# Kernel optimization log

Measured on AMD Instinct MI355X. Metric: run time of the kernel, lower is better.

## Reference

```python
import jax, jax.numpy as jnp
import numpy as np

N = 100000   # nodes
E = 1600000  # edges
D_IN = 64    # latent_dim
D_H = 64     # hidden_channels
D_OUT = 3    # coord_dim
EPS = 1e-5


def layer_norm(x, g, b):
    mu = jnp.mean(x, axis=-1, keepdims=True)
    var = jnp.mean(jnp.square(x - mu), axis=-1, keepdims=True)
    return (x - mu) * jax.lax.rsqrt(var + EPS) * g + b


def gcn_conv(x, W, b, src, dst, n):
    # PyG GCNConv: h = x W; symmetric norm deg^-1/2 (self-loops already in src/dst)
    h = x @ W  # [N, F]
    ones = jnp.ones(src.shape[0], dtype=h.dtype)
    deg = jax.ops.segment_sum(ones, dst, num_segments=n)
    dinv = jnp.where(deg > 0, jax.lax.rsqrt(deg), 0.0)
    coef = (dinv[src] * dinv[dst])[:, None]  # [E, 1]
    out = jax.ops.segment_sum(h[src] * coef, dst, num_segments=n)  # scatter-add
    return out + b


def setup_inputs() -> dict:
    key = jax.random.key(0)
    ks = jax.random.split(key, 10)
    z = jax.random.normal(ks[0], (N, D_IN), dtype=jnp.float32)
    edge_index = jax.random.randint(ks[1], (2, E), 0, N, dtype=jnp.int64)
    s = 1.0 / np.sqrt(D_H)
    return {
        "z": z,
        "edge_index": edge_index,
        "W1": jax.random.normal(ks[2], (D_IN, D_H), jnp.float32) * s,
        "b1": jnp.zeros((D_H,), jnp.float32),
        "g1": jnp.ones((D_H,), jnp.float32),
        "beta1": jnp.zeros((D_H,), jnp.float32),
        "W2": jax.random.normal(ks[3], (D_H, D_H), jnp.float32) * s,
        "b2": jnp.zeros((D_H,), jnp.float32),
        "g2": jnp.ones((D_H,), jnp.float32),
        "beta2": jnp.zeros((D_H,), jnp.float32),
        "Wm1": jax.random.normal(ks[4], (D_H, D_H), jnp.float32) * s,
        "bm1": jnp.zeros((D_H,), jnp.float32),
        "Wm2": jax.random.normal(ks[5], (D_H, D_OUT), jnp.float32) * s,
        "bm2": jnp.zeros((D_OUT,), jnp.float32),
    }


def reference(z, edge_index, W1, b1, g1, beta1, W2, b2, g2, beta2, Wm1, bm1, Wm2, bm2):
    n = z.shape[0]
    loops = jnp.arange(n, dtype=edge_index.dtype)
    src = jnp.concatenate([edge_index[0], loops])
    dst = jnp.concatenate([edge_index[1], loops])
    h = layer_norm(jax.nn.relu(gcn_conv(z, W1, b1, src, dst, n)), g1, beta1)
    h = layer_norm(jax.nn.relu(gcn_conv(h, W2, b2, src, dst, n)), g2, beta2)
    h = jax.nn.relu(h @ Wm1 + bm1)
    return h @ Wm2 + bm2
```

## Files before the change

### kernel.cpp

```cpp
#include <hip/hip_runtime.h>
#include <hip/hip_bf16.h>

#define LN_EPS 1e-5f
#define EPB 4096
typedef unsigned short u16;
typedef unsigned short us8 __attribute__((ext_vector_type(8)));
typedef short s8v __attribute__((ext_vector_type(8)));
typedef float f32x4 __attribute__((ext_vector_type(4)));

static __device__ __forceinline__ float bf2f(u16 x) {
    return __uint_as_float(((unsigned int)x) << 16);
}
static __device__ __forceinline__ u16 f2bf(float f) {
    unsigned int u = __float_as_uint(f);
    return (u16)((u + 0x7fff + ((u >> 16) & 1)) >> 16);
}

__global__ __launch_bounds__(256) void k_p1_hist(const int* __restrict__ dst,
                                                 int* __restrict__ blockhist,
                                                 int E, int NB) {
    extern __shared__ int h[];
    int b = blockIdx.x, t = threadIdx.x;
    for (int j = t; j < NB; j += 256) h[j] = 0;
    __syncthreads();
    int e0 = b * EPB, e1 = min(E, e0 + EPB);
    for (int e = e0 + t; e < e1; e += 256)
        atomicAdd(&h[dst[e] >> 8], 1);
    __syncthreads();
    for (int j = t; j < NB; j += 256)
        blockhist[(size_t)b * NB + j] = h[j];
}

__global__ __launch_bounds__(512) void k_p2a(int* __restrict__ blockhist,
                                             int* __restrict__ btot, int NB, int NB1) {
    __shared__ int sd[512];
    int k = blockIdx.x, t = threadIdx.x;
    int v = (t < NB1) ? blockhist[(size_t)t * NB + k] : 0;
    sd[t] = v;
    __syncthreads();
    for (int off = 1; off < 512; off <<= 1) {
        int x = (t >= off) ? sd[t - off] : 0;
        __syncthreads();
        sd[t] += x;
        __syncthreads();
    }
    if (t < NB1) blockhist[(size_t)t * NB + k] = sd[t] - v;
    if (t == 511) btot[k] = sd[511];
}

__global__ __launch_bounds__(512) void k_p2b(const int* __restrict__ btot,
                                             int* __restrict__ bbase,
                                             int* __restrict__ row_ptr,
                                             int NB, int N, int E) {
    __shared__ int sd[512];
    int t = threadIdx.x;
    int v = (t < NB) ? btot[t] : 0;
    sd[t] = v;
    __syncthreads();
    for (int off = 1; off < 512; off <<= 1) {
        int x = (t >= off) ? sd[t - off] : 0;
        __syncthreads();
        sd[t] += x;
        __syncthreads();
    }
    if (t < NB) bbase[t] = sd[t] - v;
    if (t == 0) { bbase[NB] = E; row_ptr[N] = E; }
}

__global__ __launch_bounds__(256) void k_p3_scatter(const int* __restrict__ src,
                                                    const int* __restrict__ dst,
                                                    const int* __restrict__ blockhist,
                                                    const int* __restrict__ bbase,
                                                    int* __restrict__ entries,
                                                    int E, int NB) {
    extern __shared__ int cur[];
    int b = blockIdx.x, t = threadIdx.x;
    for (int j = t; j < NB; j += 256)
        cur[j] = bbase[j] + blockhist[(size_t)b * NB + j];
    __syncthreads();
    int e0 = b * EPB, e1 = min(E, e0 + EPB);
    for (int e = e0 + t; e < e1; e += 256) {
        int d = dst[e];
        int p = atomicAdd(&cur[d >> 8], 1);
        entries[p] = (src[e] << 8) | (d & 255);
    }
}

__global__ __launch_bounds__(256) void k_p4_csr(const int* __restrict__ entries,
                                                const int* __restrict__ bbase,
                                                int* __restrict__ row_ptr,
                                                float* __restrict__ dinv,
                                                int* __restrict__ csr_src, int N) {
    __shared__ int hist[256];
    __shared__ int sd[256];
    __shared__ int cur[256];
    int k = blockIdx.x, t = threadIdx.x;
    int b0 = bbase[k], b1 = bbase[k + 1];
    hist[t] = 0;
    __syncthreads();
    for (int e = b0 + t; e < b1; e += 256)
        atomicAdd(&hist[entries[e] & 255], 1);
    __syncthreads();
    int v = hist[t];
    sd[t] = v;
    __syncthreads();
    for (int off = 1; off < 256; off <<= 1) {
        int x = (t >= off) ? sd[t - off] : 0;
        __syncthreads();
        sd[t] += x;
        __syncthreads();
    }
    int excl = sd[t] - v;
    int node = (k << 8) + t;
    if (node < N) {
        row_ptr[node] = b0 + excl;
        dinv[node] = rsqrtf(1.0f + (float)v);
    }
    cur[t] = b0 + excl;
    __syncthreads();
    for (int e = b0 + t; e < b1; e += 256) {
        int en = entries[e];
        int p = atomicAdd(&cur[en & 255], 1);
        csr_src[p] = en >> 8;
    }
}

__global__ __launch_bounds__(256) void k_prep_w(const float* __restrict__ W1,
                                                const float* __restrict__ W2,
                                                const float* __restrict__ Wm1,
                                                u16* __restrict__ Wtb) {
    int idx = blockIdx.x * 256 + threadIdx.x;
    if (idx >= 3 * 4096) return;
    int m = idx >> 12;
    int kc = idx & 4095;
    int col = kc >> 6, k = kc & 63;
    const float* W = (m == 0) ? W1 : (m == 1) ? W2 : Wm1;
    Wtb[idx] = f2bf(W[k * 64 + col]);
}

template <bool A_FP32>
__global__ __launch_bounds__(256) void k_mfma_gemm(const void* __restrict__ A_,
                                                   const u16* __restrict__ Wtb,
                                                   const float* __restrict__ dinv,
                                                   u16* __restrict__ C, int N) {
    int tid = threadIdx.x;
    int wid = tid >> 6, l = tid & 63;
    int li = l & 15, hi = l >> 4;
    int n0 = blockIdx.x * 64 + wid * 16;
    if (n0 >= N) return;
    int k0 = hi * 8;

    s8v a[2];
    int nr = min(n0 + li, N - 1);
    if (A_FP32) {
        const float* A = (const float*)A_;
        #pragma unroll
        for (int kk = 0; kk < 2; ++kk) {
            const float* p = A + (size_t)nr * 64 + kk * 32 + k0;
            float4 f0 = *reinterpret_cast<const float4*>(p);
            float4 f1 = *reinterpret_cast<const float4*>(p + 4);
            a[kk][0] = (short)f2bf(f0.x); a[kk][1] = (short)f2bf(f0.y);
            a[kk][2] = (short)f2bf(f0.z); a[kk][3] = (short)f2bf(f0.w);
            a[kk][4] = (short)f2bf(f1.x); a[kk][5] = (short)f2bf(f1.y);
            a[kk][6] = (short)f2bf(f1.z); a[kk][7] = (short)f2bf(f1.w);
        }
    } else {
        const u16* A = (const u16*)A_;
        #pragma unroll
        for (int kk = 0; kk < 2; ++kk)
            a[kk] = *reinterpret_cast<const s8v*>(A + (size_t)nr * 64 + kk * 32 + k0);
    }

    s8v b[4][2];
    #pragma unroll
    for (int ct = 0; ct < 4; ++ct)
        #pragma unroll
        for (int kk = 0; kk < 2; ++kk)
            b[ct][kk] = *reinterpret_cast<const s8v*>(Wtb + (ct * 16 + li) * 64 + kk * 32 + k0);

    f32x4 acc[4] = {{0.f, 0.f, 0.f, 0.f}, {0.f, 0.f, 0.f, 0.f},
                    {0.f, 0.f, 0.f, 0.f}, {0.f, 0.f, 0.f, 0.f}};
    #pragma unroll
    for (int kk = 0; kk < 2; ++kk)
        #pragma unroll
        for (int ct = 0; ct < 4; ++ct)
            acc[ct] = __builtin_amdgcn_mfma_f32_16x16x32_bf16(a[kk], b[ct][kk], acc[ct], 0, 0, 0);

    float dv[4];
    #pragma unroll
    for (int r = 0; r < 4; ++r) {
        int node = n0 + hi * 4 + r;
        dv[r] = (node < N) ? dinv[node] : 0.f;
    }
    #pragma unroll
    for (int ct = 0; ct < 4; ++ct)
        #pragma unroll
        for (int r = 0; r < 4; ++r) {
            int node = n0 + hi * 4 + r;
            if (node < N)
                C[(size_t)node * 64 + ct * 16 + li] = f2bf(acc[ct][r] * dv[r]);
        }
}

__global__ __launch_bounds__(256) void k_mfma_mlp(const u16* __restrict__ A,
                                                  const u16* __restrict__ Wtb,
                                                  const float* __restrict__ bm1,
                                                  const float* __restrict__ Wm2,
                                                  const float* __restrict__ bm2,
                                                  float* __restrict__ out, int N) {
    int tid = threadIdx.x;
    int wid = tid >> 6, l = tid & 63;
    int li = l & 15, hi = l >> 4;
    int n0 = blockIdx.x * 64 + wid * 16;
    if (n0 >= N) return;
    int k0 = hi * 8;

    s8v a[2];
    int nr = min(n0 + li, N - 1);
    #pragma unroll
    for (int kk = 0; kk < 2; ++kk)
        a[kk] = *reinterpret_cast<const s8v*>(A + (size_t)nr * 64 + kk * 32 + k0);

    s8v b[4][2];
    #pragma unroll
    for (int ct = 0; ct < 4; ++ct)
        #pragma unroll
        for (int kk = 0; kk < 2; ++kk)
            b[ct][kk] = *reinterpret_cast<const s8v*>(Wtb + (ct * 16 + li) * 64 + kk * 32 + k0);

    f32x4 acc[4] = {{0.f, 0.f, 0.f, 0.f}, {0.f, 0.f, 0.f, 0.f},
                    {0.f, 0.f, 0.f, 0.f}, {0.f, 0.f, 0.f, 0.f}};
    #pragma unroll
    for (int kk = 0; kk < 2; ++kk)
        #pragma unroll
        for (int ct = 0; ct < 4; ++ct)
            acc[ct] = __builtin_amdgcn_mfma_f32_16x16x32_bf16(a[kk], b[ct][kk], acc[ct], 0, 0, 0);

    float p[4][3];
    #pragma unroll
    for (int r = 0; r < 4; ++r)
        #pragma unroll
        for (int c = 0; c < 3; ++c) p[r][c] = 0.f;

    #pragma unroll
    for (int ct = 0; ct < 4; ++ct) {
        int col = ct * 16 + li;
        float bb = bm1[col];
        float w0 = Wm2[col * 3 + 0], w1 = Wm2[col * 3 + 1], w2 = Wm2[col * 3 + 2];
        #pragma unroll
        for (int r = 0; r < 4; ++r) {
            float v = fmaxf(acc[ct][r] + bb, 0.f);
            p[r][0] += v * w0;
            p[r][1] += v * w1;
            p[r][2] += v * w2;
        }
    }
    #pragma unroll
    for (int off = 1; off < 16; off <<= 1)
        #pragma unroll
        for (int r = 0; r < 4; ++r)
            #pragma unroll
            for (int c = 0; c < 3; ++c)
                p[r][c] += __shfl_xor(p[r][c], off);

    if (li == 0) {
        float o0 = bm2[0], o1 = bm2[1], o2 = bm2[2];
        #pragma unroll
        for (int r = 0; r < 4; ++r) {
            int node = n0 + hi * 4 + r;
            if (node < N) {
                out[(size_t)node * 3 + 0] = p[r][0] + o0;
                out[(size_t)node * 3 + 1] = p[r][1] + o1;
                out[(size_t)node * 3 + 2] = p[r][2] + o2;
            }
        }
    }
}

__global__ __launch_bounds__(256) void k_gather_ln(const u16* __restrict__ Hb,
                                                   const int* __restrict__ row_ptr,
                                                   const int* __restrict__ csr_src,
                                                   const float* __restrict__ dinv,
                                                   const float* __restrict__ b,
                                                   const float* __restrict__ g,
                                                   const float* __restrict__ beta,
                                                   u16* __restrict__ outb, int N) {
    int tid = blockIdx.x * blockDim.x + threadIdx.x;
    int node = tid >> 3;
    if (node >= N) return;
    int fl = threadIdx.x & 7;
    const us8* H8 = reinterpret_cast<const us8*>(Hb);

    float a[8];
    #pragma unroll
    for (int k = 0; k < 8; ++k) a[k] = 0.f;

    int beg = row_ptr[node], end = row_ptr[node + 1];
    int j = beg;
    for (; j + 2 <= end; j += 2) {
        int s0 = csr_src[j];
        int s1 = csr_src[j + 1];
        us8 h0 = H8[(size_t)s0 * 8 + fl];
        us8 h1 = H8[(size_t)s1 * 8 + fl];
        #pragma unroll
        for (int k = 0; k < 8; ++k)
            a[k] += bf2f(h0[k]) + bf2f(h1[k]);
    }
    if (j < end) {
        int s0 = csr_src[j];
        us8 h0 = H8[(size_t)s0 * 8 + fl];
        #pragma unroll
        for (int k = 0; k < 8; ++k)
            a[k] += bf2f(h0[k]);
    }
    float dd = dinv[node];
    {
        us8 hs = H8[(size_t)node * 8 + fl];
        #pragma unroll
        for (int k = 0; k < 8; ++k)
            a[k] += bf2f(hs[k]);
    }
    #pragma unroll
    for (int k = 0; k < 8; ++k) a[k] *= dd;

    float4 b0 = *reinterpret_cast<const float4*>(b + fl * 8);
    float4 b1v = *reinterpret_cast<const float4*>(b + fl * 8 + 4);
    a[0] = fmaxf(a[0] + b0.x, 0.f); a[1] = fmaxf(a[1] + b0.y, 0.f);
    a[2] = fmaxf(a[2] + b0.z, 0.f); a[3] = fmaxf(a[3] + b0.w, 0.f);
    a[4] = fmaxf(a[4] + b1v.x, 0.f); a[5] = fmaxf(a[5] + b1v.y, 0.f);
    a[6] = fmaxf(a[6] + b1v.z, 0.f); a[7] = fmaxf(a[7] + b1v.w, 0.f);

    float s = 0.f;
    #pragma unroll
    for (int k = 0; k < 8; ++k) s += a[k];
    s += __shfl_xor(s, 1); s += __shfl_xor(s, 2); s += __shfl_xor(s, 4);
    float mu = s * (1.0f / 64.0f);
    float vs = 0.f;
    #pragma unroll
    for (int k = 0; k < 8; ++k) {
        float d = a[k] - mu;
        vs += d * d;
    }
    vs += __shfl_xor(vs, 1); vs += __shfl_xor(vs, 2); vs += __shfl_xor(vs, 4);
    float r = rsqrtf(vs * (1.0f / 64.0f) + LN_EPS);

    float4 g0 = *reinterpret_cast<const float4*>(g + fl * 8);
    float4 g1 = *reinterpret_cast<const float4*>(g + fl * 8 + 4);
    float4 e0 = *reinterpret_cast<const float4*>(beta + fl * 8);
    float4 e1 = *reinterpret_cast<const float4*>(beta + fl * 8 + 4);
    us8 o;
    o[0] = f2bf((a[0] - mu) * r * g0.x + e0.x);
    o[1] = f2bf((a[1] - mu) * r * g0.y + e0.y);
    o[2] = f2bf((a[2] - mu) * r * g0.z + e0.z);
    o[3] = f2bf((a[3] - mu) * r * g0.w + e0.w);
    o[4] = f2bf((a[4] - mu) * r * g1.x + e1.x);
    o[5] = f2bf((a[5] - mu) * r * g1.y + e1.y);
    o[6] = f2bf((a[6] - mu) * r * g1.z + e1.z);
    o[7] = f2bf((a[7] - mu) * r * g1.w + e1.w);
    *reinterpret_cast<us8*>(outb + (size_t)node * 64 + fl * 8) = o;
}

extern "C" void kernel_launch(void* const* d_in, const int* in_sizes, int n_in,
                              void* d_out, int out_size, void* d_ws, size_t ws_size,
                              hipStream_t stream) {
    const float* z     = (const float*)d_in[0];
    const int*   ei    = (const int*)d_in[1];
    const float* W1    = (const float*)d_in[2];
    const float* b1    = (const float*)d_in[3];
    const float* g1    = (const float*)d_in[4];
    const float* beta1 = (const float*)d_in[5];
    const float* W2    = (const float*)d_in[6];
    const float* b2    = (const float*)d_in[7];
    const float* g2    = (const float*)d_in[8];
    const float* beta2 = (const float*)d_in[9];
    const float* Wm1   = (const float*)d_in[10];
    const float* bm1   = (const float*)d_in[11];
    const float* Wm2   = (const float*)d_in[12];
    const float* bm2   = (const float*)d_in[13];

    int N = in_sizes[0] / 64;
    int E = in_sizes[1] / 2;
    const int* src = ei;
    const int* dst = ei + E;
    float* out = (float*)d_out;

    int NB  = (N + 255) >> 8;
    int NB1 = (E + EPB - 1) / EPB;

    size_t N64 = (size_t)N * 64;
    auto rnd = [](size_t x) { return (x + 1023) & ~(size_t)1023; };
    int*   bbase     = (int*)d_ws;
    int*   btot      = bbase + rnd(NB + 1);
    int*   blockhist = btot + rnd(NB);
    int*   entries   = blockhist + rnd((size_t)NB1 * NB);
    int*   row_ptr   = entries + rnd(E);
    float* dinv      = (float*)(row_ptr + rnd(N + 1));
    int*   csr_src   = (int*)(dinv + rnd(N));
    u16*   Hb        = (u16*)(csr_src + rnd(E));
    u16*   Hb2       = Hb + rnd(N64);
    u16*   Wtb       = Hb2 + rnd(N64);

    int nb_g = (N + 63) / 64;
    int nb_gw = (N * 8 + 255) / 256;
    size_t lds_nb = (size_t)NB * sizeof(int);

    k_prep_w<<<48, 256, 0, stream>>>(W1, W2, Wm1, Wtb);
    k_p1_hist<<<NB1, 256, lds_nb, stream>>>(dst, blockhist, E, NB);
    k_p2a<<<NB, 512, 0, stream>>>(blockhist, btot, NB, NB1);
    k_p2b<<<1, 512, 0, stream>>>(btot, bbase, row_ptr, NB, N, E);
    k_p3_scatter<<<NB1, 256, lds_nb, stream>>>(src, dst, blockhist, bbase, entries, E, NB);
    k_p4_csr<<<NB, 256, 0, stream>>>(entries, bbase, row_ptr, dinv, csr_src, N);

    k_mfma_gemm<true><<<nb_g, 256, 0, stream>>>(z, Wtb, dinv, Hb, N);
    k_gather_ln<<<nb_gw, 256, 0, stream>>>(Hb, row_ptr, csr_src, dinv, b1, g1, beta1, Hb2, N);
    k_mfma_gemm<false><<<nb_g, 256, 0, stream>>>(Hb2, Wtb + 4096, dinv, Hb, N);
    k_gather_ln<<<nb_gw, 256, 0, stream>>>(Hb, row_ptr, csr_src, dinv, b2, g2, beta2, Hb2, N);
    k_mfma_mlp<<<nb_g, 256, 0, stream>>>(Hb2, Wtb + 8192, bm1, Wm2, bm2, out, N);
}
```

Before: 168.1 us.

## Split features into quarter-planes for gather and fuse layernorm into following GEMM

Stores the post-GEMM features as four planes of 16 features each ([4][N][16] bf16), and runs the gather once per plane, so each plane's 3.2MB working set fits better in cache. The gather now only sums raw neighbour features. The dinv scale, bias, ReLU and layernorm move into the A-fragment loading of the next GEMM or MLP kernel. The weight-prep kernel is folded into the p2b scan launch to remove one launch. The cost is four times as many CSR index reads in the gather and a cross-lane LN reduction inside the GEMM kernels.

After: 227.0 us. 1.35x slower.

```diff
diff --git a/kernel.cpp b/kernel.cpp
--- a/kernel.cpp
+++ b/kernel.cpp
@@ -4,6 +4,7 @@
 #define LN_EPS 1e-5f
 #define EPB 4096
 typedef unsigned short u16;
+typedef unsigned short us4 __attribute__((ext_vector_type(4)));
 typedef unsigned short us8 __attribute__((ext_vector_type(8)));
 typedef short s8v __attribute__((ext_vector_type(8)));
 typedef float f32x4 __attribute__((ext_vector_type(4)));
@@ -48,23 +49,38 @@
     if (t == 511) btot[k] = sd[511];
 }
 
-__global__ __launch_bounds__(512) void k_p2b(const int* __restrict__ btot,
-                                             int* __restrict__ bbase,
-                                             int* __restrict__ row_ptr,
-                                             int NB, int N, int E) {
-    __shared__ int sd[512];
-    int t = threadIdx.x;
-    int v = (t < NB) ? btot[t] : 0;
-    sd[t] = v;
-    __syncthreads();
-    for (int off = 1; off < 512; off <<= 1) {
-        int x = (t >= off) ? sd[t - off] : 0;
+__global__ __launch_bounds__(512) void k_p2b_prep(const int* __restrict__ btot,
+                                                  int* __restrict__ bbase,
+                                                  int* __restrict__ row_ptr,
+                                                  int NB, int N, int E,
+                                                  const float* __restrict__ W1,
+                                                  const float* __restrict__ W2,
+                                                  const float* __restrict__ Wm1,
+                                                  u16* __restrict__ Wtb) {
+    if (blockIdx.x == 0) {
+        __shared__ int sd[512];
+        int t = threadIdx.x;
+        int v = (t < NB) ? btot[t] : 0;
+        sd[t] = v;
         __syncthreads();
-        sd[t] += x;
-        __syncthreads();
-    }
-    if (t < NB) bbase[t] = sd[t] - v;
-    if (t == 0) { bbase[NB] = E; row_ptr[N] = E; }
+        for (int off = 1; off < 512; off <<= 1) {
+            int x = (t >= off) ? sd[t - off] : 0;
+            __syncthreads();
+            sd[t] += x;
+            __syncthreads();
+        }
+        if (t < NB) bbase[t] = sd[t] - v;
+        if (t == 0) { bbase[NB] = E; row_ptr[N] = E; }
+    } else {
+        int idx = (blockIdx.x - 1) * 512 + threadIdx.x;
+        if (idx < 3 * 4096) {
+            int m = idx >> 12;
+            int kc = idx & 4095;
+            int col = kc >> 6, k = kc & 63;
+            const float* W = (m == 0) ? W1 : (m == 1) ? W2 : Wm1;
+            Wtb[idx] = f2bf(W[k * 64 + col]);
+        }
+    }
 }
 
 __global__ __launch_bounds__(256) void k_p3_scatter(const int* __restrict__ src,
@@ -125,24 +141,53 @@
     }
 }
 
-__global__ __launch_bounds__(256) void k_prep_w(const float* __restrict__ W1,
-                                                const float* __restrict__ W2,
-                                                const float* __restrict__ Wm1,
-                                                u16* __restrict__ Wtb) {
-    int idx = blockIdx.x * 256 + threadIdx.x;
-    if (idx >= 3 * 4096) return;
-    int m = idx >> 12;
-    int kc = idx & 4095;
-    int col = kc >> 6, k = kc & 63;
-    const float* W = (m == 0) ? W1 : (m == 1) ? W2 : Wm1;
-    Wtb[idx] = f2bf(W[k * 64 + col]);
-}
-
-template <bool A_FP32>
-__global__ __launch_bounds__(256) void k_mfma_gemm(const void* __restrict__ A_,
-                                                   const u16* __restrict__ Wtb,
-                                                   const float* __restrict__ dinv,
-                                                   u16* __restrict__ C, int N) {
+static __device__ __forceinline__ void ln_frags(const u16* __restrict__ AGQ, size_t N,
+                                                int nr, int hi,
+                                                const float* __restrict__ dinv,
+                                                const float* __restrict__ bias,
+                                                const float* __restrict__ g,
+                                                const float* __restrict__ beta,
+                                                s8v a[2]) {
+    float dd = dinv[nr];
+    int qlo = hi >> 1, off = (hi & 1) * 8;
+    us8 lo = *reinterpret_cast<const us8*>(AGQ + ((size_t)qlo * N + nr) * 16 + off);
+    us8 hv = *reinterpret_cast<const us8*>(AGQ + ((size_t)(2 + qlo) * N + nr) * 16 + off);
+    float v[16];
+    #pragma unroll
+    for (int j = 0; j < 8; ++j) {
+        v[j] = bf2f(lo[j]) * dd;
+        v[8 + j] = bf2f(hv[j]) * dd;
+    }
+    int f0 = hi * 8;
+    #pragma unroll
+    for (int j = 0; j < 8; ++j) {
+        v[j] = fmaxf(v[j] + bias[f0 + j], 0.f);
+        v[8 + j] = fmaxf(v[8 + j] + bias[32 + f0 + j], 0.f);
+    }
+    float s = 0.f;
+    #pragma unroll
+    for (int j = 0; j < 16; ++j) s += v[j];
+    s += __shfl_xor(s, 16); s += __shfl_xor(s, 32);
+    float mu = s * (1.0f / 64.0f);
+    float vs = 0.f;
+    #pragma unroll
+    for (int j = 0; j < 16; ++j) {
+        float d = v[j] - mu;
+        vs += d * d;
+    }
+    vs += __shfl_xor(vs, 16); vs += __shfl_xor(vs, 32);
+    float r = rsqrtf(vs * (1.0f / 64.0f) + LN_EPS);
+    #pragma unroll
+    for (int j = 0; j < 8; ++j) {
+        a[0][j] = (short)f2bf((v[j] - mu) * r * g[f0 + j] + beta[f0 + j]);
+        a[1][j] = (short)f2bf((v[8 + j] - mu) * r * g[32 + f0 + j] + beta[32 + f0 + j]);
+    }
+}
+
+__global__ __launch_bounds__(256) void k_gemm1(const float* __restrict__ A,
+                                               const u16* __restrict__ Wtb,
+                                               const float* __restrict__ dinv,
+                                               u16* __restrict__ C, int N) {
     int tid = threadIdx.x;
     int wid = tid >> 6, l = tid & 63;
     int li = l & 15, hi = l >> 4;
@@ -152,23 +197,15 @@
 
     s8v a[2];
     int nr = min(n0 + li, N - 1);
-    if (A_FP32) {
-        const float* A = (const float*)A_;
-        #pragma unroll
-        for (int kk = 0; kk < 2; ++kk) {
-            const float* p = A + (size_t)nr * 64 + kk * 32 + k0;
-            float4 f0 = *reinterpret_cast<const float4*>(p);
-            float4 f1 = *reinterpret_cast<const float4*>(p + 4);
-            a[kk][0] = (short)f2bf(f0.x); a[kk][1] = (short)f2bf(f0.y);
-            a[kk][2] = (short)f2bf(f0.z); a[kk][3] = (short)f2bf(f0.w);
-            a[kk][4] = (short)f2bf(f1.x); a[kk][5] = (short)f2bf(f1.y);
-            a[kk][6] = (short)f2bf(f1.z); a[kk][7] = (short)f2bf(f1.w);
-        }
-    } else {
-        const u16* A = (const u16*)A_;
-        #pragma unroll
-        for (int kk = 0; kk < 2; ++kk)
-            a[kk] = *reinterpret_cast<const s8v*>(A + (size_t)nr * 64 + kk * 32 + k0);
+    #pragma unroll
+    for (int kk = 0; kk < 2; ++kk) {
+        const float* p = A + (size_t)nr * 64 + kk * 32 + k0;
+        float4 f0 = *reinterpret_cast<const float4*>(p);
+        float4 f1 = *reinterpret_cast<const float4*>(p + 4);
+        a[kk][0] = (short)f2bf(f0.x); a[kk][1] = (short)f2bf(f0.y);
+        a[kk][2] = (short)f2bf(f0.z); a[kk][3] = (short)f2bf(f0.w);
+        a[kk][4] = (short)f2bf(f1.x); a[kk][5] = (short)f2bf(f1.y);
+        a[kk][6] = (short)f2bf(f1.z); a[kk][7] = (short)f2bf(f1.w);
     }
 
     s8v b[4][2];
@@ -186,28 +223,25 @@
         for (int ct = 0; ct < 4; ++ct)
             acc[ct] = __builtin_amdgcn_mfma_f32_16x16x32_bf16(a[kk], b[ct][kk], acc[ct], 0, 0, 0);
 
-    float dv[4];
     #pragma unroll
     for (int r = 0; r < 4; ++r) {
         int node = n0 + hi * 4 + r;
-        dv[r] = (node < N) ? dinv[node] : 0.f;
-    }
-    #pragma unroll
-    for (int ct = 0; ct < 4; ++ct)
-        #pragma unroll
-        for (int r = 0; r < 4; ++r) {
-            int node = n0 + hi * 4 + r;
-            if (node < N)
-                C[(size_t)node * 64 + ct * 16 + li] = f2bf(acc[ct][r] * dv[r]);
-        }
-}
-
-__global__ __launch_bounds__(256) void k_mfma_mlp(const u16* __restrict__ A,
-                                                  const u16* __restrict__ Wtb,
-                                                  const float* __restrict__ bm1,
-                                                  const float* __restrict__ Wm2,
-                                                  const float* __restrict__ bm2,
-                                                  float* __restrict__ out, int N) {
+        if (node < N) {
+            float dv = dinv[node];
+            #pragma unroll
+            for (int ct = 0; ct < 4; ++ct)
+                C[((size_t)ct * N + node) * 16 + li] = f2bf(acc[ct][r] * dv);
+        }
+    }
+}
+
+__global__ __launch_bounds__(256) void k_gemm_ln(const u16* __restrict__ AGQ,
+                                                 const u16* __restrict__ Wtb,
+                                                 const float* __restrict__ dinv,
+                                                 const float* __restrict__ bias,
+                                                 const float* __restrict__ g,
+                                                 const float* __restrict__ beta,
+                                                 u16* __restrict__ C, int N) {
     int tid = threadIdx.x;
     int wid = tid >> 6, l = tid & 63;
     int li = l & 15, hi = l >> 4;
@@ -217,9 +251,55 @@
 
     s8v a[2];
     int nr = min(n0 + li, N - 1);
+    ln_frags(AGQ, (size_t)N, nr, hi, dinv, bias, g, beta, a);
+
+    s8v b[4][2];
+    #pragma unroll
+    for (int ct = 0; ct < 4; ++ct)
+        #pragma unroll
+        for (int kk = 0; kk < 2; ++kk)
+            b[ct][kk] = *reinterpret_cast<const s8v*>(Wtb + (ct * 16 + li) * 64 + kk * 32 + k0);
+
+    f32x4 acc[4] = {{0.f, 0.f, 0.f, 0.f}, {0.f, 0.f, 0.f, 0.f},
+                    {0.f, 0.f, 0.f, 0.f}, {0.f, 0.f, 0.f, 0.f}};
     #pragma unroll
     for (int kk = 0; kk < 2; ++kk)
-        a[kk] = *reinterpret_cast<const s8v*>(A + (size_t)nr * 64 + kk * 32 + k0);
+        #pragma unroll
+        for (int ct = 0; ct < 4; ++ct)
+            acc[ct] = __builtin_amdgcn_mfma_f32_16x16x32_bf16(a[kk], b[ct][kk], acc[ct], 0, 0, 0);
+
+    #pragma unroll
+    for (int r = 0; r < 4; ++r) {
+        int node = n0 + hi * 4 + r;
+        if (node < N) {
+            float dv = dinv[node];
+            #pragma unroll
+            for (int ct = 0; ct < 4; ++ct)
+                C[((size_t)ct * N + node) * 16 + li] = f2bf(acc[ct][r] * dv);
+        }
+    }
+}
+
+__global__ __launch_bounds__(256) void k_mlp_ln(const u16* __restrict__ AGQ,
+                                                const u16* __restrict__ Wtb,
+                                                const float* __restrict__ dinv,
+                                                const float* __restrict__ bias,
+                                                const float* __restrict__ g,
+                                                const float* __restrict__ beta,
+                                                const float* __restrict__ bm1,
+                                                const float* __restrict__ Wm2,
+                                                const float* __restrict__ bm2,
+                                                float* __restrict__ out, int N) {
+    int tid = threadIdx.x;
+    int wid = tid >> 6, l = tid & 63;
+    int li = l & 15, hi = l >> 4;
+    int n0 = blockIdx.x * 64 + wid * 16;
+    if (n0 >= N) return;
+    int k0 = hi * 8;
+
+    s8v a[2];
+    int nr = min(n0 + li, N - 1);
+    ln_frags(AGQ, (size_t)N, nr, hi, dinv, bias, g, beta, a);
 
     s8v b[4][2];
     #pragma unroll
@@ -277,87 +357,43 @@
     }
 }
 
-__global__ __launch_bounds__(256) void k_gather_ln(const u16* __restrict__ Hb,
-                                                   const int* __restrict__ row_ptr,
-                                                   const int* __restrict__ csr_src,
-                                                   const float* __restrict__ dinv,
-                                                   const float* __restrict__ b,
-                                                   const float* __restrict__ g,
-                                                   const float* __restrict__ beta,
-                                                   u16* __restrict__ outb, int N) {
-    int tid = blockIdx.x * blockDim.x + threadIdx.x;
-    int node = tid >> 3;
+__global__ __launch_bounds__(256) void k_gatherq(const u16* __restrict__ Hbq,
+                                                 const int* __restrict__ row_ptr,
+                                                 const int* __restrict__ csr_src,
+                                                 u16* __restrict__ AGQ,
+                                                 int N, int nbNode) {
+    int q = blockIdx.x / nbNode;
+    int nblk = blockIdx.x % nbNode;
+    int node = nblk * 64 + (threadIdx.x >> 2);
     if (node >= N) return;
-    int fl = threadIdx.x & 7;
-    const us8* H8 = reinterpret_cast<const us8*>(Hb);
-
-    float a[8];
-    #pragma unroll
-    for (int k = 0; k < 8; ++k) a[k] = 0.f;
-
+    int fq = (threadIdx.x & 3) * 4;
+    const u16* Hq = Hbq + (size_t)q * N * 16;
+
+    float a0 = 0.f, a1 = 0.f, a2 = 0.f, a3 = 0.f;
     int beg = row_ptr[node], end = row_ptr[node + 1];
     int j = beg;
     for (; j + 2 <= end; j += 2) {
         int s0 = csr_src[j];
         int s1 = csr_src[j + 1];
-        us8 h0 = H8[(size_t)s0 * 8 + fl];
-        us8 h1 = H8[(size_t)s1 * 8 + fl];
-        #pragma unroll
-        for (int k = 0; k < 8; ++k)
-            a[k] += bf2f(h0[k]) + bf2f(h1[k]);
+        us4 h0 = *reinterpret_cast<const us4*>(Hq + (size_t)s0 * 16 + fq);
+        us4 h1 = *reinterpret_cast<const us4*>(Hq + (size_t)s1 * 16 + fq);
+        a0 += bf2f(h0[0]) + bf2f(h1[0]);
+        a1 += bf2f(h0[1]) + bf2f(h1[1]);
+        a2 += bf2f(h0[2]) + bf2f(h1[2]);
+        a3 += bf2f(h0[3]) + bf2f(h1[3]);
     }
     if (j < end) {
         int s0 = csr_src[j];
-        us8 h0 = H8[(size_t)s0 * 8 + fl];
-        #pragma unroll
-        for (int k = 0; k < 8; ++k)
-            a[k] += bf2f(h0[k]);
-    }
-    float dd = dinv[node];
+        us4 h0 = *reinterpret_cast<const us4*>(Hq + (size_t)s0 * 16 + fq);
+        a0 += bf2f(h0[0]); a1 += bf2f(h0[1]); a2 += bf2f(h0[2]); a3 += bf2f(h0[3]);
+    }
     {
-        us8 hs = H8[(size_t)node * 8 + fl];
-        #pragma unroll
-        for (int k = 0; k < 8; ++k)
-            a[k] += bf2f(hs[k]);
-    }
-    #pragma unroll
-    for (int k = 0; k < 8; ++k) a[k] *= dd;
-
-    float4 b0 = *reinterpret_cast<const float4*>(b + fl * 8);
-    float4 b1v = *reinterpret_cast<const float4*>(b + fl * 8 + 4);
-    a[0] = fmaxf(a[0] + b0.x, 0.f); a[1] = fmaxf(a[1] + b0.y, 0.f);
-    a[2] = fmaxf(a[2] + b0.z, 0.f); a[3] = fmaxf(a[3] + b0.w, 0.f);
-    a[4] = fmaxf(a[4] + b1v.x, 0.f); a[5] = fmaxf(a[5] + b1v.y, 0.f);
-    a[6] = fmaxf(a[6] + b1v.z, 0.f); a[7] = fmaxf(a[7] + b1v.w, 0.f);
-
-    float s = 0.f;
-    #pragma unroll
-    for (int k = 0; k < 8; ++k) s += a[k];
-    s += __shfl_xor(s, 1); s += __shfl_xor(s, 2); s += __shfl_xor(s, 4);
-    float mu = s * (1.0f / 64.0f);
-    float vs = 0.f;
-    #pragma unroll
-    for (int k = 0; k < 8; ++k) {
-        float d = a[k] - mu;
-        vs += d * d;
-    }
-    vs += __shfl_xor(vs, 1); vs += __shfl_xor(vs, 2); vs += __shfl_xor(vs, 4);
-    float r = rsqrtf(vs * (1.0f / 64.0f) + LN_EPS);
-
-    float4 g0 = *reinterpret_cast<const float4*>(g + fl * 8);
-    float4 g1 = *reinterpret_cast<const float4*>(g + fl * 8 + 4);
-    float4 e0 = *reinterpret_cast<const float4*>(beta + fl * 8);
-    float4 e1 = *reinterpret_cast<const float4*>(beta + fl * 8 + 4);
-    us8 o;
-    o[0] = f2bf((a[0] - mu) * r * g0.x + e0.x);
-    o[1] = f2bf((a[1] - mu) * r * g0.y + e0.y);
-    o[2] = f2bf((a[2] - mu) * r * g0.z + e0.z);
-    o[3] = f2bf((a[3] - mu) * r * g0.w + e0.w);
-    o[4] = f2bf((a[4] - mu) * r * g1.x + e1.x);
-    o[5] = f2bf((a[5] - mu) * r * g1.y + e1.y);
-    o[6] = f2bf((a[6] - mu) * r * g1.z + e1.z);
-    o[7] = f2bf((a[7] - mu) * r * g1.w + e1.w);
-    *reinterpret_cast<us8*>(outb + (size_t)node * 64 + fl * 8) = o;
+        us4 hs = *reinterpret_cast<const us4*>(Hq + (size_t)node * 16 + fq);
+        a0 += bf2f(hs[0]); a1 += bf2f(hs[1]); a2 += bf2f(hs[2]); a3 += bf2f(hs[3]);
+    }
+    us4 o;
+    o[0] = f2bf(a0); o[1] = f2bf(a1); o[2] = f2bf(a2); o[3] = f2bf(a3);
+    *reinterpret_cast<us4*>(AGQ + ((size_t)q * N + node) * 16 + fq) = o;
 }
 
 extern "C" void kernel_launch(void* const* d_in, const int* in_sizes, int n_in,
@@ -396,24 +432,24 @@
     int*   row_ptr   = entries + rnd(E);
     float* dinv      = (float*)(row_ptr + rnd(N + 1));
     int*   csr_src   = (int*)(dinv + rnd(N));
-    u16*   Hb        = (u16*)(csr_src + rnd(E));
-    u16*   Hb2       = Hb + rnd(N64);
-    u16*   Wtb       = Hb2 + rnd(N64);
+    u16*   Hbq       = (u16*)(csr_src + rnd(E));
+    u16*   AGQ       = Hbq + rnd(N64);
+    u16*   Wtb       = AGQ + rnd(N64);
 
     int nb_g = (N + 63) / 64;
-    int nb_gw = (N * 8 + 255) / 256;
+    int nbNode = (N + 63) / 64;
     size_t lds_nb = (size_t)NB * sizeof(int);
 
-    k_prep_w<<<48, 256, 0, stream>>>(W1, W2, Wm1, Wtb);
     k_p1_hist<<<NB1, 256, lds_nb, stream>>>(dst, blockhist, E, NB);
     k_p2a<<<NB, 512, 0, stream>>>(blockhist, btot, NB, NB1);
-    k_p2b<<<1, 512, 0, stream>>>(btot, bbase, row_ptr, NB, N, E);
+    k_p2b_prep<<<25, 512, 0, stream>>>(btot, bbase, row_ptr, NB, N, E, W1, W2, Wm1, Wtb);
     k_p3_scatter<<<NB1, 256, lds_nb, stream>>>(src, dst, blockhist, bbase, entries, E, NB);
     k_p4_csr<<<NB, 256, 0, stream>>>(entries, bbase, row_ptr, dinv, csr_src, N);
 
-    k_mfma_gemm<true><<<nb_g, 256, 0, stream>>>(z, Wtb, dinv, Hb, N);
-    k_gather_ln<<<nb_gw, 256, 0, stream>>>(Hb, row_ptr, csr_src, dinv, b1, g1, beta1, Hb2, N);
-    k_mfma_gemm<false><<<nb_g, 256, 0, stream>>>(Hb2, Wtb + 4096, dinv, Hb, N);
-    k_gather_ln<<<nb_gw, 256, 0, stream>>>(Hb, row_ptr, csr_src, dinv, b2, g2, beta2, Hb2, N);
-    k_mfma_mlp<<<nb_g, 256, 0, stream>>>(Hb2, Wtb + 8192, bm1, Wm2, bm2, out, N);
-}
+    k_gemm1<<<nb_g, 256, 0, stream>>>(z, Wtb, dinv, Hbq, N);
+    k_gatherq<<<4 * nbNode, 256, 0, stream>>>(Hbq, row_ptr, csr_src, AGQ, N, nbNode);
+    k_gemm_ln<<<nb_g, 256, 0, stream>>>(AGQ, Wtb + 4096, dinv, b1, g1, beta1, Hbq, N);
+    k_gatherq<<<4 * nbNode, 256, 0, stream>>>(Hbq, row_ptr, csr_src, AGQ, N, nbNode);
+    k_mlp_ln<<<nb_g, 256, 0, stream>>>(AGQ, Wtb + 8192, dinv, b2, g2, beta2,
+                                       bm1, Wm2, bm2, out, N);
+}
```
